# Kernel optimization log

Measured on AMD Instinct MI355X. Metric: run time of the kernel, lower is better.

Reference implementation:

```python
import jax, jax.numpy as jnp
import numpy as np

N = 500000          # num_nodes; module's broadcast requires num_edges == num_nodes
E = 500000
F_IN = 128          # node_features
H = 128             # hidden_dim
LAT = 32            # latent_dim
NT = 16             # num_node_types
ET = 4              # num_edge_types


def _lin_init(key, fan_in, fan_out):
    k1, k2 = jax.random.split(key)
    s = 1.0 / np.sqrt(fan_in)
    W = jax.random.uniform(k1, (fan_in, fan_out), jnp.float32, -s, s)
    b = jax.random.uniform(k2, (fan_out,), jnp.float32, -s, s)
    return W, b


def setup_inputs() -> dict:
    key = jax.random.key(0)
    ks = jax.random.split(key, 12)
    x = jax.random.normal(ks[0], (N, F_IN), jnp.float32)
    edge_index = jax.random.randint(ks[1], (2, E), 0, N, jnp.int64)
    eps = jax.random.normal(ks[2], (1, LAT), jnp.float32)
    W1, b1 = _lin_init(ks[3], F_IN, H)      # encoder conv1
    W2, b2 = _lin_init(ks[4], H, H)         # encoder conv2
    Wmu, bmu = _lin_init(ks[5], H, LAT)     # fc_mu (out_channels//2 = latent_dim)
    Wlv, blv = _lin_init(ks[6], H, LAT)     # fc_logvar
    Wn, bn = _lin_init(ks[7], LAT, NT)      # decoder node_type_proj
    We1, be1 = _lin_init(ks[8], 2 * LAT, H) # decoder edge_mlp[0]
    We2, be2 = _lin_init(ks[9], H, ET)      # decoder edge_mlp[2]
    return dict(x=x, edge_index=edge_index, eps=eps,
                W1=W1, b1=b1, W2=W2, b2=b2, Wmu=Wmu, bmu=bmu, Wlv=Wlv, blv=blv,
                Wn=Wn, bn=bn, We1=We1, be1=be1, We2=We2, be2=be2)


def _gcn_conv(x, row, col, W, b):
    # out = linear(x); per-edge symmetric degree norm; scatter aggregation.
    out = x @ W + b                                   # [N, C]
    n = x.shape[0]
    deg = jnp.zeros((n,), x.dtype).at[row].add(1.0)   # out-degree via scatter_add
    dis = jnp.where(deg > 0, jax.lax.rsqrt(deg), 0.0) # deg^-0.5, inf -> 0
    norm = dis[row] * dis[col]                        # [E]; E == N by module structure
    out = out * norm[:, None]                         # broadcast over rows (E == N)
    agg = jnp.zeros_like(out).at[row].add(out[col])   # gather + index_add
    return agg


def reference(x, edge_index, eps, W1, b1, W2, b2, Wmu, bmu, Wlv, blv,
              Wn, bn, We1, be1, We2, be2):
    row, col = edge_index[0], edge_index[1]
    # --- encoder ---
    h = jax.nn.relu(_gcn_conv(x, row, col, W1, b1))
    h = jax.nn.relu(_gcn_conv(h, row, col, W2, b2))
    g = jnp.mean(h, axis=0, keepdims=True)            # [1, H]
    mu = g @ Wmu + bmu                                # [1, LAT]
    logvar = g @ Wlv + blv                            # [1, LAT]
    # --- reparameterize ---
    z = mu + eps * jnp.exp(0.5 * logvar)              # [1, LAT]
    # --- decoder ---
    node_logits = z @ Wn + bn                         # [1, NT]
    # z has one row; z[row]/z[col] clamp to z[0] -> equivalent to broadcast
    zz = jnp.concatenate([z, z], axis=-1)             # [1, 2*LAT]
    ef = jnp.broadcast_to(zz, (row.shape[0], 2 * z.shape[-1]))
    eh = jax.nn.relu(ef @ We1 + be1)                  # [E, H]
    edge_logits = eh @ We2 + be2                      # [E, ET]
    return (node_logits, edge_logits, mu, logvar)
```

## Files before the change

### kernel.cpp

```cpp
#include <hip/hip_runtime.h>
#include <hip/hip_bf16.h>


#define FDIM 128

typedef __attribute__((ext_vector_type(8))) short bf16x8;
typedef __attribute__((ext_vector_type(8))) unsigned short ushort8;
typedef __attribute__((ext_vector_type(4))) float f32x4;

static __device__ __forceinline__ unsigned short f2bf(float f) {
  union { float f; unsigned u; } v; v.f = f;
  unsigned r = v.u + 0x7FFFu + ((v.u >> 16) & 1u);
  return (unsigned short)(r >> 16);
}
static __device__ __forceinline__ float bf2f(unsigned short b) {
  union { unsigned u; float f; } v; v.u = ((unsigned)b) << 16;
  return v.f;
}

__global__ void prep_w(const float* __restrict__ W, unsigned short* __restrict__ img) {
  int idx = blockIdx.x * 256 + threadIdx.x;
  int n = idx & 127, k = idx >> 7;
  unsigned short b = f2bf(W[(size_t)k * 128 + n]);
  int byte = n * 256 + ((k * 2) ^ ((n & 7) << 4));
  img[byte >> 1] = b;
}

__global__ void count_deg(const int* __restrict__ row, float* __restrict__ deg, int E) {
  int e = blockIdx.x * blockDim.x + threadIdx.x;
  if (e < E) atomicAdd(&deg[row[e]], 1.0f);
}

__global__ void mknorm(const float* __restrict__ dis, const int* __restrict__ row,
                       const int* __restrict__ col, float* __restrict__ nrm, int E) {
  int i = blockIdx.x * blockDim.x + threadIdx.x;
  if (i < E) nrm[i] = dis[row[i]] * dis[col[i]];
}

#define SCAN_B 256

__global__ __launch_bounds__(SCAN_B) void scan1(const float* __restrict__ deg,
                                                float* __restrict__ dis,
                                                int* __restrict__ rs,
                                                int* __restrict__ part, int N) {
  __shared__ int s[SCAN_B];
  int t = threadIdx.x, i = blockIdx.x * SCAN_B + t;
  float d = (i < N) ? deg[i] : 0.f;
  if (i < N) dis[i] = d > 0.f ? rsqrtf(d) : 0.f;
  int v = (int)d;
  s[t] = v;
  __syncthreads();
  for (int off = 1; off < SCAN_B; off <<= 1) {
    int x = (t >= off) ? s[t - off] : 0;
    __syncthreads();
    s[t] += x;
    __syncthreads();
  }
  if (i < N) rs[i] = s[t] - v;
  if (t == SCAN_B - 1) part[blockIdx.x] = s[t];
}

__global__ __launch_bounds__(SCAN_B) void scan2(int* __restrict__ part, int nblk) {
  __shared__ int s[SCAN_B];
  int t = threadIdx.x;
  int carry = 0;
  for (int base = 0; base < nblk; base += SCAN_B) {
    int i = base + t;
    int v = (i < nblk) ? part[i] : 0;
    s[t] = v;
    __syncthreads();
    for (int off = 1; off < SCAN_B; off <<= 1) {
      int x = (t >= off) ? s[t - off] : 0;
      __syncthreads();
      s[t] += x;
      __syncthreads();
    }
    if (i < nblk) part[i] = carry + s[t] - v;
    int tot = s[SCAN_B - 1];
    __syncthreads();
    carry += tot;
  }
}

__global__ __launch_bounds__(SCAN_B) void scan3(int* __restrict__ rs, const int* __restrict__ part,
                                                int* __restrict__ cursor, int N, int E) {
  int t = threadIdx.x, i = blockIdx.x * SCAN_B + t;
  if (i < N) {
    int v = rs[i] + part[blockIdx.x];
    rs[i] = v;
    cursor[i] = v;
  }
  if (i == 0) rs[N] = E;
}

__global__ void fill_csr(const int* __restrict__ row, const int* __restrict__ col,
                         int* __restrict__ cursor, int* __restrict__ csr_col, int E) {
  int e = blockIdx.x * blockDim.x + threadIdx.x;
  if (e < E) {
    int p = atomicAdd(&cursor[row[e]], 1);
    csr_col[p] = col[e];
  }
}

template <bool BF16IN>
__global__ __launch_bounds__(256) void gemm_scale(const void* __restrict__ in_,
                                                  const unsigned short* __restrict__ Wimg,
                                                  const float* __restrict__ bias,
                                                  const float* __restrict__ nrm,
                                                  unsigned short* __restrict__ out,
                                                  int N, int ntiles) {
  __shared__ unsigned short Wt[128 * 128 / 2 * 1];
  (void)Wt;
  __shared__ unsigned short Wlds[128 * 128];

  const int tid = threadIdx.x;
  const int wave = tid >> 6, lane = tid & 63;
  const int l15 = lane & 15, lhi = lane >> 4;

  {
    const char* gsrc = (const char*)Wimg;
    char* ldst = (char*)Wlds;
#pragma unroll
    for (int j = 0; j < 8; ++j) {
      int off = (wave * 8 + j) * 1024;
      __builtin_amdgcn_global_load_lds(
          (const __attribute__((address_space(1))) unsigned int*)(gsrc + off + lane * 16),
          (__attribute__((address_space(3))) unsigned int*)(ldst + off),
          16, 0, 0);
    }
  }
  __syncthreads();

  const int swz = (l15 & 7) << 4;

  for (int tile = blockIdx.x; tile < ntiles; tile += gridDim.x) {
    const int row = tile * 64 + wave * 16 + l15;
    const bool valid = row < N;

    bf16x8 afrag[4];
    if (BF16IN) {
      const unsigned short* in = (const unsigned short*)in_ + (size_t)row * 128 + lhi * 8;
#pragma unroll
      for (int kt = 0; kt < 4; ++kt) {
        bf16x8 f = {};
        if (valid) f = *(const bf16x8*)(in + kt * 32);
        afrag[kt] = f;
      }
    } else {
      const float* in = (const float*)in_ + (size_t)row * 128 + lhi * 8;
#pragma unroll
      for (int kt = 0; kt < 4; ++kt) {
        float4 lo = make_float4(0.f, 0.f, 0.f, 0.f), hi = lo;
        if (valid) {
          lo = *(const float4*)(in + kt * 32);
          hi = *(const float4*)(in + kt * 32 + 4);
        }
        bf16x8 f;
        f[0] = (short)f2bf(lo.x); f[1] = (short)f2bf(lo.y);
        f[2] = (short)f2bf(lo.z); f[3] = (short)f2bf(lo.w);
        f[4] = (short)f2bf(hi.x); f[5] = (short)f2bf(hi.y);
        f[6] = (short)f2bf(hi.z); f[7] = (short)f2bf(hi.w);
        afrag[kt] = f;
      }
    }

    f32x4 acc[8] = {};
#pragma unroll
    for (int kt = 0; kt < 4; ++kt) {
      const int kswz = (kt * 64 + lhi * 16) ^ swz;
#pragma unroll
      for (int ct = 0; ct < 8; ++ct) {
        const int bbyte = (ct * 16 + l15) * 256 + kswz;
        bf16x8 bfrag = *(const bf16x8*)((const char*)Wlds + bbyte);
        acc[ct] = __builtin_amdgcn_mfma_f32_16x16x32_bf16(bfrag, afrag[kt], acc[ct], 0, 0, 0);
      }
    }

    const float nv = valid ? nrm[row] : 0.f;
    unsigned short* orow = out + (size_t)row * 128 + lhi * 4;
#pragma unroll
    for (int ct = 0; ct < 8; ++ct) {
      float4 bv = *(const float4*)(bias + ct * 16 + lhi * 4);
      if (valid) {
        ushort4 o;
        o.x = f2bf((acc[ct][0] + bv.x) * nv);
        o.y = f2bf((acc[ct][1] + bv.y) * nv);
        o.z = f2bf((acc[ct][2] + bv.z) * nv);
        o.w = f2bf((acc[ct][3] + bv.w) * nv);
        *(ushort4*)(orow + ct * 16) = o;
      }
    }
  }
}

__global__ __launch_bounds__(256) void aggregate_h(const unsigned short* __restrict__ scaled,
                                                   const int* __restrict__ rs,
                                                   const int* __restrict__ csr_col,
                                                   unsigned short* __restrict__ h1, int N) {
  int gt = blockIdx.x * 256 + threadIdx.x;
  int node = gt >> 4, lane = gt & 15;
  if (node >= N) return;
  int s = rs[node], e = rs[node + 1];
  float a[8] = {};
  for (int j = s; j < e; ++j) {
    int c = csr_col[j];
    ushort8 v = ((const ushort8*)(scaled + (size_t)c * 128))[lane];
#pragma unroll
    for (int i = 0; i < 8; ++i) a[i] += bf2f(v[i]);
  }
  ushort8 o;
#pragma unroll
  for (int i = 0; i < 8; ++i) o[i] = f2bf(fmaxf(a[i], 0.f));
  ((ushort8*)(h1 + (size_t)node * 128))[lane] = o;
}

__global__ __launch_bounds__(256) void aggregate_mean(const unsigned short* __restrict__ scaled,
                                                      const int* __restrict__ rs,
                                                      const int* __restrict__ csr_col,
                                                      float* __restrict__ g, int N) {
  __shared__ float sd[16][16][8];
  int tid = threadIdx.x, grp = tid >> 4, lane = tid & 15;
  float g8[8] = {};
  for (int node = blockIdx.x * 16 + grp; node < N; node += gridDim.x * 16) {
    int s = rs[node], e = rs[node + 1];
    float a[8] = {};
    for (int j = s; j < e; ++j) {
      int c = csr_col[j];
      ushort8 v = ((const ushort8*)(scaled + (size_t)c * 128))[lane];
#pragma unroll
      for (int i = 0; i < 8; ++i) a[i] += bf2f(v[i]);
    }
#pragma unroll
    for (int i = 0; i < 8; ++i) g8[i] += fmaxf(a[i], 0.f);
  }
#pragma unroll
  for (int i = 0; i < 8; ++i) sd[grp][lane][i] = g8[i];
  __syncthreads();
  if (tid < 128) {
    int l = tid >> 3, j = tid & 7;
    float s = 0.f;
#pragma unroll
    for (int q = 0; q < 16; ++q) s += sd[q][l][j];
    atomicAdd(&g[l * 8 + j], s);
  }
}

__global__ void tail_kernel(const float* __restrict__ g, const float* __restrict__ eps,
                            const float* __restrict__ Wmu, const float* __restrict__ bmu,
                            const float* __restrict__ Wlv, const float* __restrict__ blv,
                            const float* __restrict__ Wn, const float* __restrict__ bn,
                            const float* __restrict__ We1, const float* __restrict__ be1,
                            const float* __restrict__ We2, const float* __restrict__ be2,
                            float* __restrict__ out, float* __restrict__ el4,
                            int N, int E) {
  __shared__ float gm[128], zs[32], eh[128];
  int t = threadIdx.x;
  gm[t] = g[t] / (float)N;
  __syncthreads();
  if (t < 32) {
    float mu = bmu[t], lv = blv[t];
#pragma unroll 8
    for (int k = 0; k < 128; ++k) {
      mu = fmaf(gm[k], Wmu[k * 32 + t], mu);
      lv = fmaf(gm[k], Wlv[k * 32 + t], lv);
    }
    zs[t] = mu + eps[t] * expf(0.5f * lv);
    out[16 + 4 * (size_t)E + t] = mu;
    out[16 + 4 * (size_t)E + 32 + t] = lv;
  }
  __syncthreads();
  if (t < 16) {
    float v = bn[t];
#pragma unroll
    for (int j = 0; j < 32; ++j) v = fmaf(zs[j], Wn[j * 16 + t], v);
    out[t] = v;
  }
  {
    float v = be1[t];
#pragma unroll 8
    for (int j = 0; j < 32; ++j)
      v = fmaf(zs[j], We1[j * 128 + t] + We1[(j + 32) * 128 + t], v);
    eh[t] = fmaxf(v, 0.f);
  }
  __syncthreads();
  if (t < 4) {
    float v = be2[t];
#pragma unroll 8
    for (int k = 0; k < 128; ++k) v = fmaf(eh[k], We2[k * 4 + t], v);
    el4[t] = v;
  }
}

__global__ __launch_bounds__(256) void bcast_edges(const float* __restrict__ el4,
                                                   float* __restrict__ out16, int E) {
  int i = blockIdx.x * 256 + threadIdx.x;
  if (i < E) {
    float4 v = *(const float4*)el4;
    ((float4*)out16)[i] = v;
  }
}

extern "C" void kernel_launch(void* const* d_in, const int* in_sizes, int n_in,
                              void* d_out, int out_size, void* d_ws, size_t ws_size,
                              hipStream_t stream) {
  const float* x   = (const float*)d_in[0];
  const int*   ei  = (const int*)d_in[1];
  const float* eps = (const float*)d_in[2];
  const float* W1  = (const float*)d_in[3];
  const float* b1  = (const float*)d_in[4];
  const float* W2  = (const float*)d_in[5];
  const float* b2  = (const float*)d_in[6];
  const float* Wmu = (const float*)d_in[7];
  const float* bmu = (const float*)d_in[8];
  const float* Wlv = (const float*)d_in[9];
  const float* blv = (const float*)d_in[10];
  const float* Wn  = (const float*)d_in[11];
  const float* bn  = (const float*)d_in[12];
  const float* We1 = (const float*)d_in[13];
  const float* be1 = (const float*)d_in[14];
  const float* We2 = (const float*)d_in[15];
  const float* be2 = (const float*)d_in[16];

  const int N = in_sizes[0] / FDIM;
  const int E = in_sizes[1] / 2;
  const int* row = ei;
  const int* col = ei + E;
  float* out = (float*)d_out;

  const int nscan = (N + SCAN_B - 1) / SCAN_B;
  const int ntiles = (N + 63) / 64;

  char* ws = (char*)d_ws;
  size_t off = 0;
  float* deg    = (float*)(ws + off); off += (size_t)N * 4;
  float* dis    = (float*)(ws + off); off += (size_t)N * 4;
  float* nrm    = (float*)(ws + off); off += (size_t)E * 4;
  int*   rs     = (int*)(ws + off);   off += ((size_t)N + 1) * 4;
  int*   cursor = (int*)(ws + off);   off += (size_t)N * 4;
  int*   part   = (int*)(ws + off);   off += (size_t)nscan * 4;
  int*   csrcol = (int*)(ws + off);   off += (size_t)E * 4;
  float* g      = (float*)(ws + off); off += 128 * 4;
  float* el4    = (float*)(ws + off); off += 4 * 4;
  off = (off + 1023) & ~(size_t)1023;
  unsigned short* Wimg1 = (unsigned short*)(ws + off); off += 16384 * 2;
  unsigned short* Wimg2 = (unsigned short*)(ws + off); off += 16384 * 2;
  off = (off + 1023) & ~(size_t)1023;
  unsigned short* scaled = (unsigned short*)(ws + off); off += (size_t)N * FDIM * 2;
  off = (off + 1023) & ~(size_t)1023;
  unsigned short* h1     = (unsigned short*)(ws + off); off += (size_t)N * FDIM * 2;

  hipMemsetAsync(deg, 0, (size_t)N * 4, stream);
  hipMemsetAsync(g, 0, 128 * 4, stream);

  prep_w<<<64, 256, 0, stream>>>(W1, Wimg1);
  prep_w<<<64, 256, 0, stream>>>(W2, Wimg2);
  count_deg<<<(E + 255) / 256, 256, 0, stream>>>(row, deg, E);
  scan1<<<nscan, SCAN_B, 0, stream>>>(deg, dis, rs, part, N);
  scan2<<<1, SCAN_B, 0, stream>>>(part, nscan);
  scan3<<<nscan, SCAN_B, 0, stream>>>(rs, part, cursor, N, E);
  mknorm<<<(E + 255) / 256, 256, 0, stream>>>(dis, row, col, nrm, E);
  fill_csr<<<(E + 255) / 256, 256, 0, stream>>>(row, col, cursor, csrcol, E);

  gemm_scale<false><<<1280, 256, 0, stream>>>(x, Wimg1, b1, nrm, scaled, N, ntiles);
  aggregate_h<<<((size_t)N * 16 + 255) / 256, 256, 0, stream>>>(scaled, rs, csrcol, h1, N);

  gemm_scale<true><<<1280, 256, 0, stream>>>(h1, Wimg2, b2, nrm, scaled, N, ntiles);
  aggregate_mean<<<1024, 256, 0, stream>>>(scaled, rs, csrcol, g, N);

  tail_kernel<<<1, 128, 0, stream>>>(g, eps, Wmu, bmu, Wlv, blv, Wn, bn,
                                     We1, be1, We2, be2, out, el4, N, E);
  bcast_edges<<<(E + 255) / 256, 256, 0, stream>>>(el4, out + 16, E);
}
```

Measured before the change: 740.2 us.

## Double-buffer layer-2 GEMM A tiles via LDS, swizzle h1, batch aggregation per group

The layer-2 GEMM now streams 64-row tiles of h1 into a double-buffered LDS staging area with global_load_lds, prefetching the next tile while computing the current one. aggregate_h writes h1 rows in an XOR-swizzled chunk order so these LDS reads avoid bank conflicts. Both aggregation kernels now have each 16-lane group process four consecutive nodes, which exposes more independent gathers per thread. The norm computation is folded into the CSR fill kernel, and the two weight-prep launches are merged into one. In exchange the kernel uses more LDS, which may lower occupancy, and aggregation load balance gets coarser.

```diff
diff --git a/kernel.cpp b/kernel.cpp
--- a/kernel.cpp
+++ b/kernel.cpp
@@ -18,23 +18,18 @@
   return v.f;
 }
 
-__global__ void prep_w(const float* __restrict__ W, unsigned short* __restrict__ img) {
+__global__ void prep_w(const float* __restrict__ W1, const float* __restrict__ W2,
+                       unsigned short* __restrict__ img1, unsigned short* __restrict__ img2) {
   int idx = blockIdx.x * 256 + threadIdx.x;
   int n = idx & 127, k = idx >> 7;
-  unsigned short b = f2bf(W[(size_t)k * 128 + n]);
   int byte = n * 256 + ((k * 2) ^ ((n & 7) << 4));
-  img[byte >> 1] = b;
+  img1[byte >> 1] = f2bf(W1[(size_t)k * 128 + n]);
+  img2[byte >> 1] = f2bf(W2[(size_t)k * 128 + n]);
 }
 
 __global__ void count_deg(const int* __restrict__ row, float* __restrict__ deg, int E) {
   int e = blockIdx.x * blockDim.x + threadIdx.x;
   if (e < E) atomicAdd(&deg[row[e]], 1.0f);
-}
-
-__global__ void mknorm(const float* __restrict__ dis, const int* __restrict__ row,
-                       const int* __restrict__ col, float* __restrict__ nrm, int E) {
-  int i = blockIdx.x * blockDim.x + threadIdx.x;
-  if (i < E) nrm[i] = dis[row[i]] * dis[col[i]];
 }
 
 #define SCAN_B 256
@@ -93,24 +88,24 @@
   if (i == 0) rs[N] = E;
 }
 
-__global__ void fill_csr(const int* __restrict__ row, const int* __restrict__ col,
-                         int* __restrict__ cursor, int* __restrict__ csr_col, int E) {
+__global__ void fill_csr_norm(const int* __restrict__ row, const int* __restrict__ col,
+                              const float* __restrict__ dis, int* __restrict__ cursor,
+                              int* __restrict__ csr_col, float* __restrict__ nrm, int E) {
   int e = blockIdx.x * blockDim.x + threadIdx.x;
   if (e < E) {
-    int p = atomicAdd(&cursor[row[e]], 1);
-    csr_col[p] = col[e];
-  }
-}
-
-template <bool BF16IN>
-__global__ __launch_bounds__(256) void gemm_scale(const void* __restrict__ in_,
-                                                  const unsigned short* __restrict__ Wimg,
-                                                  const float* __restrict__ bias,
-                                                  const float* __restrict__ nrm,
-                                                  unsigned short* __restrict__ out,
-                                                  int N, int ntiles) {
-  __shared__ unsigned short Wt[128 * 128 / 2 * 1];
-  (void)Wt;
+    int r = row[e], c = col[e];
+    nrm[e] = dis[r] * dis[c];
+    int p = atomicAdd(&cursor[r], 1);
+    csr_col[p] = c;
+  }
+}
+
+__global__ __launch_bounds__(256) void gemm1_scale(const float* __restrict__ in,
+                                                   const unsigned short* __restrict__ Wimg,
+                                                   const float* __restrict__ bias,
+                                                   const float* __restrict__ nrm,
+                                                   unsigned short* __restrict__ out,
+                                                   int N, int ntiles) {
   __shared__ unsigned short Wlds[128 * 128];
 
   const int tid = threadIdx.x;
@@ -138,22 +133,14 @@
     const bool valid = row < N;
 
     bf16x8 afrag[4];
-    if (BF16IN) {
-      const unsigned short* in = (const unsigned short*)in_ + (size_t)row * 128 + lhi * 8;
-#pragma unroll
-      for (int kt = 0; kt < 4; ++kt) {
-        bf16x8 f = {};
-        if (valid) f = *(const bf16x8*)(in + kt * 32);
-        afrag[kt] = f;
-      }
-    } else {
-      const float* in = (const float*)in_ + (size_t)row * 128 + lhi * 8;
+    {
+      const float* inp = in + (size_t)row * 128 + lhi * 8;
 #pragma unroll
       for (int kt = 0; kt < 4; ++kt) {
         float4 lo = make_float4(0.f, 0.f, 0.f, 0.f), hi = lo;
         if (valid) {
-          lo = *(const float4*)(in + kt * 32);
-          hi = *(const float4*)(in + kt * 32 + 4);
+          lo = *(const float4*)(inp + kt * 32);
+          hi = *(const float4*)(inp + kt * 32 + 4);
         }
         bf16x8 f;
         f[0] = (short)f2bf(lo.x); f[1] = (short)f2bf(lo.y);
@@ -193,25 +180,153 @@
   }
 }
 
+__global__ __launch_bounds__(256) void gemm2_scale(const unsigned short* __restrict__ h1,
+                                                   const unsigned short* __restrict__ Wimg,
+                                                   const float* __restrict__ bias,
+                                                   const float* __restrict__ nrm,
+                                                   unsigned short* __restrict__ out,
+                                                   int N, int ntiles) {
+  __shared__ unsigned short Wlds[128 * 128];
+  __shared__ __align__(16) unsigned short Alds[2][64 * 128];
+
+  const int tid = threadIdx.x;
+  const int wave = tid >> 6, lane = tid & 63;
+  const int l15 = lane & 15, lhi = lane >> 4;
+
+  {
+    const char* gsrc = (const char*)Wimg;
+    char* ldst = (char*)Wlds;
+#pragma unroll
+    for (int j = 0; j < 8; ++j) {
+      int off = (wave * 8 + j) * 1024;
+      __builtin_amdgcn_global_load_lds(
+          (const __attribute__((address_space(1))) unsigned int*)(gsrc + off + lane * 16),
+          (__attribute__((address_space(3))) unsigned int*)(ldst + off),
+          16, 0, 0);
+    }
+  }
+
+  const int swz = (l15 & 7) << 4;
+  const int t0 = blockIdx.x;
+
+  auto stageA = [&](int t, int b) {
+    const char* src = (const char*)h1 + (size_t)t * 16384 + tid * 16;
+    char* dst = (char*)Alds[b] + tid * 16;
+#pragma unroll
+    for (int j = 0; j < 4; ++j) {
+      __builtin_amdgcn_global_load_lds(
+          (const __attribute__((address_space(1))) unsigned int*)(src + j * 4096),
+          (__attribute__((address_space(3))) unsigned int*)(dst + j * 4096),
+          16, 0, 0);
+    }
+  };
+
+  if (t0 < ntiles) stageA(t0, 0);
+  int cur = 0;
+
+  for (int tile = t0; tile < ntiles; tile += gridDim.x) {
+    __syncthreads();
+    int tn = tile + gridDim.x;
+    if (tn < ntiles) stageA(tn, cur ^ 1);
+
+    const int arow = wave * 16 + l15;
+    const char* Ab = (const char*)Alds[cur];
+    bf16x8 afrag[4];
+#pragma unroll
+    for (int kt = 0; kt < 4; ++kt)
+      afrag[kt] = *(const bf16x8*)(Ab + arow * 256 + ((kt * 64 + lhi * 16) ^ ((arow & 7) << 4)));
+
+    f32x4 acc[8] = {};
+#pragma unroll
+    for (int kt = 0; kt < 4; ++kt) {
+      const int kswz = (kt * 64 + lhi * 16) ^ swz;
+#pragma unroll
+      for (int ct = 0; ct < 8; ++ct) {
+        const int bbyte = (ct * 16 + l15) * 256 + kswz;
+        bf16x8 bfrag = *(const bf16x8*)((const char*)Wlds + bbyte);
+        acc[ct] = __builtin_amdgcn_mfma_f32_16x16x32_bf16(bfrag, afrag[kt], acc[ct], 0, 0, 0);
+      }
+    }
+
+    const int row = tile * 64 + arow;
+    const bool valid = row < N;
+    const float nv = valid ? nrm[row] : 0.f;
+    unsigned short* orow = out + (size_t)row * 128 + lhi * 4;
+#pragma unroll
+    for (int ct = 0; ct < 8; ++ct) {
+      float4 bv = *(const float4*)(bias + ct * 16 + lhi * 4);
+      if (valid) {
+        ushort4 o;
+        o.x = f2bf((acc[ct][0] + bv.x) * nv);
+        o.y = f2bf((acc[ct][1] + bv.y) * nv);
+        o.z = f2bf((acc[ct][2] + bv.z) * nv);
+        o.w = f2bf((acc[ct][3] + bv.w) * nv);
+        *(ushort4*)(orow + ct * 16) = o;
+      }
+    }
+    __syncthreads();
+    cur ^= 1;
+  }
+}
+
+#define ACC_ADD(A, v) { A[0]+=bf2f(v[0]); A[1]+=bf2f(v[1]); A[2]+=bf2f(v[2]); A[3]+=bf2f(v[3]); \
+                        A[4]+=bf2f(v[4]); A[5]+=bf2f(v[5]); A[6]+=bf2f(v[6]); A[7]+=bf2f(v[7]); }
+
 __global__ __launch_bounds__(256) void aggregate_h(const unsigned short* __restrict__ scaled,
                                                    const int* __restrict__ rs,
                                                    const int* __restrict__ csr_col,
                                                    unsigned short* __restrict__ h1, int N) {
   int gt = blockIdx.x * 256 + threadIdx.x;
-  int node = gt >> 4, lane = gt & 15;
-  if (node >= N) return;
-  int s = rs[node], e = rs[node + 1];
-  float a[8] = {};
-  for (int j = s; j < e; ++j) {
+  int grp = gt >> 4, lane = gt & 15;
+  int n0 = grp * 4;
+  if (n0 >= N) return;
+  int e0 = rs[n0];
+  int e1 = rs[min(n0 + 1, N)];
+  int e2 = rs[min(n0 + 2, N)];
+  int e3 = rs[min(n0 + 3, N)];
+  int e4 = rs[min(n0 + 4, N)];
+
+  float A0[8] = {}, A1[8] = {}, A2[8] = {}, A3[8] = {};
+  for (int j = e0; j < e1; ++j) {
     int c = csr_col[j];
     ushort8 v = ((const ushort8*)(scaled + (size_t)c * 128))[lane];
-#pragma unroll
-    for (int i = 0; i < 8; ++i) a[i] += bf2f(v[i]);
-  }
+    ACC_ADD(A0, v)
+  }
+  for (int j = e1; j < e2; ++j) {
+    int c = csr_col[j];
+    ushort8 v = ((const ushort8*)(scaled + (size_t)c * 128))[lane];
+    ACC_ADD(A1, v)
+  }
+  for (int j = e2; j < e3; ++j) {
+    int c = csr_col[j];
+    ushort8 v = ((const ushort8*)(scaled + (size_t)c * 128))[lane];
+    ACC_ADD(A2, v)
+  }
+  for (int j = e3; j < e4; ++j) {
+    int c = csr_col[j];
+    ushort8 v = ((const ushort8*)(scaled + (size_t)c * 128))[lane];
+    ACC_ADD(A3, v)
+  }
+
   ushort8 o;
 #pragma unroll
-  for (int i = 0; i < 8; ++i) o[i] = f2bf(fmaxf(a[i], 0.f));
-  ((ushort8*)(h1 + (size_t)node * 128))[lane] = o;
+  for (int i = 0; i < 8; ++i) o[i] = f2bf(fmaxf(A0[i], 0.f));
+  ((ushort8*)(h1 + (size_t)n0 * 128))[lane ^ (n0 & 7)] = o;
+  if (n0 + 1 < N) {
+#pragma unroll
+    for (int i = 0; i < 8; ++i) o[i] = f2bf(fmaxf(A1[i], 0.f));
+    ((ushort8*)(h1 + (size_t)(n0 + 1) * 128))[lane ^ ((n0 + 1) & 7)] = o;
+  }
+  if (n0 + 2 < N) {
+#pragma unroll
+    for (int i = 0; i < 8; ++i) o[i] = f2bf(fmaxf(A2[i], 0.f));
+    ((ushort8*)(h1 + (size_t)(n0 + 2) * 128))[lane ^ ((n0 + 2) & 7)] = o;
+  }
+  if (n0 + 3 < N) {
+#pragma unroll
+    for (int i = 0; i < 8; ++i) o[i] = f2bf(fmaxf(A3[i], 0.f));
+    ((ushort8*)(h1 + (size_t)(n0 + 3) * 128))[lane ^ ((n0 + 3) & 7)] = o;
+  }
 }
 
 __global__ __launch_bounds__(256) void aggregate_mean(const unsigned short* __restrict__ scaled,
@@ -220,21 +335,41 @@
                                                       float* __restrict__ g, int N) {
   __shared__ float sd[16][16][8];
   int tid = threadIdx.x, grp = tid >> 4, lane = tid & 15;
-  float g8[8] = {};
-  for (int node = blockIdx.x * 16 + grp; node < N; node += gridDim.x * 16) {
-    int s = rs[node], e = rs[node + 1];
-    float a[8] = {};
-    for (int j = s; j < e; ++j) {
+  float acc[8] = {};
+  const int step = gridDim.x * 16 * 4;
+  for (int n0 = (blockIdx.x * 16 + grp) * 4; n0 < N; n0 += step) {
+    int e0 = rs[n0];
+    int e1 = rs[min(n0 + 1, N)];
+    int e2 = rs[min(n0 + 2, N)];
+    int e3 = rs[min(n0 + 3, N)];
+    int e4 = rs[min(n0 + 4, N)];
+    float A0[8] = {}, A1[8] = {}, A2[8] = {}, A3[8] = {};
+    for (int j = e0; j < e1; ++j) {
       int c = csr_col[j];
       ushort8 v = ((const ushort8*)(scaled + (size_t)c * 128))[lane];
-#pragma unroll
-      for (int i = 0; i < 8; ++i) a[i] += bf2f(v[i]);
-    }
-#pragma unroll
-    for (int i = 0; i < 8; ++i) g8[i] += fmaxf(a[i], 0.f);
-  }
-#pragma unroll
-  for (int i = 0; i < 8; ++i) sd[grp][lane][i] = g8[i];
+      ACC_ADD(A0, v)
+    }
+    for (int j = e1; j < e2; ++j) {
+      int c = csr_col[j];
+      ushort8 v = ((const ushort8*)(scaled + (size_t)c * 128))[lane];
+      ACC_ADD(A1, v)
+    }
+    for (int j = e2; j < e3; ++j) {
+      int c = csr_col[j];
+      ushort8 v = ((const ushort8*)(scaled + (size_t)c * 128))[lane];
+      ACC_ADD(A2, v)
+    }
+    for (int j = e3; j < e4; ++j) {
+      int c = csr_col[j];
+      ushort8 v = ((const ushort8*)(scaled + (size_t)c * 128))[lane];
+      ACC_ADD(A3, v)
+    }
+#pragma unroll
+    for (int i = 0; i < 8; ++i)
+      acc[i] += fmaxf(A0[i], 0.f) + fmaxf(A1[i], 0.f) + fmaxf(A2[i], 0.f) + fmaxf(A3[i], 0.f);
+  }
+#pragma unroll
+  for (int i = 0; i < 8; ++i) sd[grp][lane][i] = acc[i];
   __syncthreads();
   if (tid < 128) {
     int l = tid >> 3, j = tid & 7;
@@ -348,23 +483,22 @@
   unsigned short* scaled = (unsigned short*)(ws + off); off += (size_t)N * FDIM * 2;
   off = (off + 1023) & ~(size_t)1023;
   unsigned short* h1     = (unsigned short*)(ws + off); off += (size_t)N * FDIM * 2;
+  off += 16384;
 
   hipMemsetAsync(deg, 0, (size_t)N * 4, stream);
   hipMemsetAsync(g, 0, 128 * 4, stream);
 
-  prep_w<<<64, 256, 0, stream>>>(W1, Wimg1);
-  prep_w<<<64, 256, 0, stream>>>(W2, Wimg2);
+  prep_w<<<64, 256, 0, stream>>>(W1, W2, Wimg1, Wimg2);
   count_deg<<<(E + 255) / 256, 256, 0, stream>>>(row, deg, E);
   scan1<<<nscan, SCAN_B, 0, stream>>>(deg, dis, rs, part, N);
   scan2<<<1, SCAN_B, 0, stream>>>(part, nscan);
   scan3<<<nscan, SCAN_B, 0, stream>>>(rs, part, cursor, N, E);
-  mknorm<<<(E + 255) / 256, 256, 0, stream>>>(dis, row, col, nrm, E);
-  fill_csr<<<(E + 255) / 256, 256, 0, stream>>>(row, col, cursor, csrcol, E);
-
-  gemm_scale<false><<<1280, 256, 0, stream>>>(x, Wimg1, b1, nrm, scaled, N, ntiles);
-  aggregate_h<<<((size_t)N * 16 + 255) / 256, 256, 0, stream>>>(scaled, rs, csrcol, h1, N);
-
-  gemm_scale<true><<<1280, 256, 0, stream>>>(h1, Wimg2, b2, nrm, scaled, N, ntiles);
+  fill_csr_norm<<<(E + 255) / 256, 256, 0, stream>>>(row, col, dis, cursor, csrcol, nrm, E);
+
+  gemm1_scale<<<1280, 256, 0, stream>>>(x, Wimg1, b1, nrm, scaled, N, ntiles);
+  aggregate_h<<<((size_t)(N + 3) / 4 * 16 + 255) / 256, 256, 0, stream>>>(scaled, rs, csrcol, h1, N);
+
+  gemm2_scale<<<1280, 256, 0, stream>>>(h1, Wimg2, b2, nrm, scaled, N, ntiles);
   aggregate_mean<<<1024, 256, 0, stream>>>(scaled, rs, csrcol, g, N);
 
   tail_kernel<<<1, 128, 0, stream>>>(g, eps, Wmu, bmu, Wlv, blv, Wn, bn,
```

After: 720.1 us. -2.7%, faster.
